# Kernel tuning notes

Measured on AMD Instinct MI355X. Metric: run time of the kernel, lower is better.

Reference implementation:

```python
import jax, jax.numpy as jnp
import numpy as np

B, T, K = 512, 512, 128
START, STOP = K - 2, K - 1
NEG = -10000.0


def setup_inputs() -> dict:
    key = jax.random.key(0)
    k1, k2, k3 = jax.random.split(key, 3)
    feats = jax.random.normal(k1, (B, T, K), dtype=jnp.float32)
    # gold tags exclude START/STOP
    tags = jax.random.randint(k2, (B, T), 0, K - 2)
    transitions = jax.random.normal(k3, (K, K), dtype=jnp.float32)
    # __init__ pins: transitions[START, :] = -10000 ; transitions[:, STOP] = -10000
    transitions = transitions.at[START, :].set(NEG).at[:, STOP].set(NEG)
    return {"feats": feats, "tags": tags, "transitions": transitions}


def _forward_alg(feats, transitions):
    # feats: [B, T, K]; CRF partition function via log-space semiring scan
    Bb, Tt, Kk = feats.shape
    alpha0 = jnp.full((Bb, Kk), NEG, dtype=feats.dtype).at[:, START].set(0.0)

    def step(alpha, feat):  # alpha: [B, K_prev], feat: [B, K_next]
        # score[b, next, prev] = alpha[b, prev] + T[next, prev] + feat[b, next]
        s = alpha[:, None, :] + transitions[None, :, :] + feat[:, :, None]
        return jax.nn.logsumexp(s, axis=-1), None

    alpha, _ = jax.lax.scan(step, alpha0, jnp.swapaxes(feats, 0, 1))
    return jax.nn.logsumexp(alpha + transitions[STOP], axis=-1)  # [B]


def _score_sentence(feats, tags, transitions):
    # score of the gold path, fully vectorized over time
    Bb = feats.shape[0]
    start = jnp.full((Bb, 1), START, dtype=tags.dtype)
    ext = jnp.concatenate([start, tags], axis=1)  # [B, T+1]
    trans_score = transitions[ext[:, 1:], ext[:, :-1]].sum(axis=1)  # [B]
    emit_score = jnp.take_along_axis(feats, tags[:, :, None], axis=2)[..., 0].sum(axis=1)
    return trans_score + emit_score + transitions[STOP, ext[:, -1]]


def reference(feats, tags, transitions):
    # neg_log_likelihood: mean over batch of (log Z - gold path score)
    forward_score = _forward_alg(feats, transitions)
    gold_score = _score_sentence(feats, tags, transitions)
    return jnp.sum(forward_score - gold_score) / feats.shape[0]
```

## Files before the change

kernel.cpp:

```cpp
#include <hip/hip_runtime.h>
#include <math.h>

#define Bb 512
#define Tt 512
#define Kk 128
#define NSTART 126
#define NSTOP  127
#define PW 32
#define NTHR 256

static constexpr float LOG2E = 1.4426950408889634f;
static constexpr float LN2   = 0.6931471805599453f;

__device__ __forceinline__ float fexp2(float x) {
  return __builtin_amdgcn_exp2f(x);
}
__device__ __forceinline__ float flog2(float x) {
  return __builtin_amdgcn_logf(x);
}

__global__ __launch_bounds__(NTHR, 2) void crf_nll_lin2(
    const float* __restrict__ feats,
    const int*   __restrict__ tags,
    const float* __restrict__ trans,
    float* __restrict__ part)
{
  const int b   = blockIdx.x;
  const int tid = threadIdx.x;
  const int q   = tid & 3;
  const int nb  = tid >> 2;
  const int n0  = nb;
  const int n1  = nb + 64;
  const int w   = tid >> 6;

  __shared__ __align__(16) float aL[2][4][Kk];
  __shared__ float red[4];

  float E0[PW], E1[PW];
  {
    const float* t0 = trans + (size_t)n0 * Kk + q * PW;
    const float* t1 = trans + (size_t)n1 * Kk + q * PW;
    #pragma unroll
    for (int j = 0; j < PW; j += 4) {
      float4 v0 = *(const float4*)(t0 + j);
      float4 v1 = *(const float4*)(t1 + j);
      E0[j+0] = fexp2(v0.x * LOG2E);
      E0[j+1] = fexp2(v0.y * LOG2E);
      E0[j+2] = fexp2(v0.z * LOG2E);
      E0[j+3] = fexp2(v0.w * LOG2E);
      E1[j+0] = fexp2(v1.x * LOG2E);
      E1[j+1] = fexp2(v1.y * LOG2E);
      E1[j+2] = fexp2(v1.z * LOG2E);
      E1[j+3] = fexp2(v1.w * LOG2E);
    }
  }
  #pragma unroll
  for (int j = 0; j < PW; ++j) {
    asm volatile("" : "+v"(E0[j]), "+v"(E1[j]));
  }

  aL[0][q][(n0 - 8*q) & (Kk-1)] = (n0 == NSTART) ? 1.0f : 0.0f;
  aL[0][q][(n1 - 8*q) & (Kk-1)] = (n1 == NSTART) ? 1.0f : 0.0f;
  __syncthreads();

  const float* fb = feats + (size_t)b * Tt * Kk;
  float C2 = 0.0f;
  float f0 = fb[n0], f1 = fb[n1];

  for (int t = 0; t < Tt; ++t) {
    const int cur = t & 1;
    float f0n = 0.f, f1n = 0.f;
    if (t + 1 < Tt) {
      f0n = fb[(size_t)(t + 1) * Kk + n0];
      f1n = fb[(size_t)(t + 1) * Kk + n1];
    }

    const float* ap = &aL[cur][q][q * 24];
    float a0=0.f,a1=0.f,a2=0.f,a3=0.f, c0=0.f,c1=0.f,c2=0.f,c3=0.f;
    #pragma unroll
    for (int j4 = 0; j4 < PW/4; ++j4) {
      const float4 av = *(const float4*)(ap + j4*4);
      a0 = fmaf(E0[4*j4+0], av.x, a0);
      a1 = fmaf(E0[4*j4+1], av.y, a1);
      a2 = fmaf(E0[4*j4+2], av.z, a2);
      a3 = fmaf(E0[4*j4+3], av.w, a3);
      c0 = fmaf(E1[4*j4+0], av.x, c0);
      c1 = fmaf(E1[4*j4+1], av.y, c1);
      c2 = fmaf(E1[4*j4+2], av.z, c2);
      c3 = fmaf(E1[4*j4+3], av.w, c3);
    }
    float s0 = (a0 + a1) + (a2 + a3);
    float s1 = (c0 + c1) + (c2 + c3);
    s0 += __shfl_xor(s0, 1, 64);
    s0 += __shfl_xor(s0, 2, 64);
    s1 += __shfl_xor(s1, 1, 64);
    s1 += __shfl_xor(s1, 2, 64);
    float y0 = fexp2(f0 * LOG2E) * s0;
    float y1 = fexp2(f1 * LOG2E) * s1;

    if ((t & 3) == 3) {
      float m = fmaxf(y0, y1);
      m = fmaxf(m, __shfl_xor(m, 4, 64));
      m = fmaxf(m, __shfl_xor(m, 8, 64));
      m = fmaxf(m, __shfl_xor(m, 16, 64));
      m = fmaxf(m, __shfl_xor(m, 32, 64));
      if ((tid & 63) == 0) red[w] = m;
      __syncthreads();
      m = fmaxf(fmaxf(red[0], red[1]), fmaxf(red[2], red[3]));
      C2 += flog2(m);
      float inv = 1.0f / m;
      y0 *= inv; y1 *= inv;
    }

    const int nxt = cur ^ 1;
    aL[nxt][q][(n0 - 8*q) & (Kk-1)] = y0;
    aL[nxt][q][(n1 - 8*q) & (Kk-1)] = y1;
    __syncthreads();
    f0 = f0n; f1 = f1n;
  }

  float v = 0.0f;
  if (tid < Kk) {
    float es = fexp2(trans[(size_t)NSTOP * Kk + tid] * LOG2E);
    v = aL[0][0][tid] * es;
  }
  #pragma unroll
  for (int off = 32; off >= 1; off >>= 1) v += __shfl_xor(v, off, 64);
  if ((tid & 63) == 0) red[w] = v;
  __syncthreads();
  const float S = (red[0] + red[1]) + (red[2] + red[3]);
  const float fwd = LN2 * (C2 + flog2(S));

  __syncthreads();
  const int* tg = tags + (size_t)b * Tt;
  float g = 0.0f;
  #pragma unroll
  for (int k2 = 0; k2 < Tt / NTHR; ++k2) {
    const int tt  = tid + k2 * NTHR;
    const int curt = tg[tt];
    const int prv  = (tt == 0) ? NSTART : tg[tt - 1];
    g += trans[(size_t)curt * Kk + prv] + fb[(size_t)tt * Kk + curt];
  }
  if (tid == 0) g += trans[(size_t)NSTOP * Kk + tg[Tt - 1]];
  #pragma unroll
  for (int off = 32; off >= 1; off >>= 1) g += __shfl_xor(g, off, 64);
  if ((tid & 63) == 0) red[w] = g;
  __syncthreads();
  const float gold = (red[0] + red[1]) + (red[2] + red[3]);

  if (tid == 0) part[b] = fwd - gold;
}

__global__ __launch_bounds__(256) void reduce_mean_kernel(
    const float* __restrict__ part, float* __restrict__ out)
{
  __shared__ float buf[4];
  const int tid = threadIdx.x;
  float v = part[tid] + part[tid + 256];
  #pragma unroll
  for (int off = 32; off >= 1; off >>= 1) v += __shfl_xor(v, off, 64);
  if ((tid & 63) == 0) buf[tid >> 6] = v;
  __syncthreads();
  if (tid == 0)
    out[0] = (buf[0] + buf[1] + buf[2] + buf[3]) * (1.0f / (float)Bb);
}

extern "C" void kernel_launch(void* const* d_in, const int* in_sizes, int n_in,
                              void* d_out, int out_size, void* d_ws, size_t ws_size,
                              hipStream_t stream) {
  const float* feats = (const float*)d_in[0];
  const int*   tags  = (const int*)d_in[1];
  const float* trans = (const float*)d_in[2];
  float* part = (float*)d_ws;

  crf_nll_lin2<<<dim3(Bb), dim3(NTHR), 0, stream>>>(feats, tags, trans, part);
  reduce_mean_kernel<<<dim3(1), dim3(256), 0, stream>>>(part, (float*)d_out);
}
```

Before: 256.5 us.

## Halve threads per sequence, four next-states per thread, DPP quad reductions

Shrinks each block from 256 to 128 threads (2 waves), so each thread now owns four next-tag rows of exp(transitions) in registers (128 floats) instead of two. Each LDS float4 load of alpha is now reused across four rows, and the per-step barrier spans only two waves. The quad partial-sum reduction switches from ds_swizzle-style shuffles to DPP quad_perm adds, and the division becomes a hardware reciprocal. The cost is much higher register pressure and fewer waves per sequence, so the latency of the serial recurrence is less hidden.

```diff
diff --git a/kernel.cpp b/kernel.cpp
--- a/kernel.cpp
+++ b/kernel.cpp
@@ -6,20 +6,29 @@
 #define Kk 128
 #define NSTART 126
 #define NSTOP  127
+#define NTHR 128
+#define RN 4
+#define QS 4
 #define PW 32
-#define NTHR 256
 
 static constexpr float LOG2E = 1.4426950408889634f;
 static constexpr float LN2   = 0.6931471805599453f;
 
-__device__ __forceinline__ float fexp2(float x) {
-  return __builtin_amdgcn_exp2f(x);
+__device__ __forceinline__ float fexp2(float x) { return __builtin_amdgcn_exp2f(x); }
+__device__ __forceinline__ float flog2(float x) { return __builtin_amdgcn_logf(x); }
+__device__ __forceinline__ float frcp (float x) { return __builtin_amdgcn_rcpf(x); }
+
+template <int CTRL>
+__device__ __forceinline__ float dpp_qp_add(float s) {
+  union { float f; int i; } a, r;
+  a.f = s;
+  r.i = __builtin_amdgcn_update_dpp(a.i, a.i, CTRL, 0xf, 0xf, false);
+  return s + r.f;
 }
-__device__ __forceinline__ float flog2(float x) {
-  return __builtin_amdgcn_logf(x);
-}
+#define QP_XOR1 0xB1
+#define QP_XOR2 0x4E
 
-__global__ __launch_bounds__(NTHR, 2) void crf_nll_lin2(
+__global__ __launch_bounds__(NTHR, 1) void crf_nll_lin3(
     const float* __restrict__ feats,
     const int*   __restrict__ tags,
     const float* __restrict__ trans,
@@ -29,114 +38,118 @@
   const int tid = threadIdx.x;
   const int q   = tid & 3;
   const int nb  = tid >> 2;
-  const int n0  = nb;
-  const int n1  = nb + 64;
   const int w   = tid >> 6;
 
-  __shared__ __align__(16) float aL[2][4][Kk];
-  __shared__ float red[4];
+  __shared__ __align__(16) float aL[2][QS][Kk];
+  __shared__ float red[2];
 
-  float E0[PW], E1[PW];
-  {
-    const float* t0 = trans + (size_t)n0 * Kk + q * PW;
-    const float* t1 = trans + (size_t)n1 * Kk + q * PW;
+  float E[RN][PW];
+  #pragma unroll
+  for (int r = 0; r < RN; ++r) {
+    const float* tr = trans + (size_t)(nb + 32*r) * Kk + q * PW;
     #pragma unroll
     for (int j = 0; j < PW; j += 4) {
-      float4 v0 = *(const float4*)(t0 + j);
-      float4 v1 = *(const float4*)(t1 + j);
-      E0[j+0] = fexp2(v0.x * LOG2E);
-      E0[j+1] = fexp2(v0.y * LOG2E);
-      E0[j+2] = fexp2(v0.z * LOG2E);
-      E0[j+3] = fexp2(v0.w * LOG2E);
-      E1[j+0] = fexp2(v1.x * LOG2E);
-      E1[j+1] = fexp2(v1.y * LOG2E);
-      E1[j+2] = fexp2(v1.z * LOG2E);
-      E1[j+3] = fexp2(v1.w * LOG2E);
+      float4 v = *(const float4*)(tr + j);
+      E[r][j+0] = fexp2(v.x * LOG2E);
+      E[r][j+1] = fexp2(v.y * LOG2E);
+      E[r][j+2] = fexp2(v.z * LOG2E);
+      E[r][j+3] = fexp2(v.w * LOG2E);
     }
   }
   #pragma unroll
-  for (int j = 0; j < PW; ++j) {
-    asm volatile("" : "+v"(E0[j]), "+v"(E1[j]));
-  }
+  for (int r = 0; r < RN; ++r)
+    #pragma unroll
+    for (int j = 0; j < PW; ++j)
+      asm volatile("" : "+v"(E[r][j]));
 
-  aL[0][q][(n0 - 8*q) & (Kk-1)] = (n0 == NSTART) ? 1.0f : 0.0f;
-  aL[0][q][(n1 - 8*q) & (Kk-1)] = (n1 == NSTART) ? 1.0f : 0.0f;
+  int wi[RN];
+  #pragma unroll
+  for (int r = 0; r < RN; ++r) wi[r] = ((nb + 32*r) - 8*q) & (Kk - 1);
+
+  #pragma unroll
+  for (int r = 0; r < RN; ++r)
+    aL[0][q][wi[r]] = ((nb + 32*r) == NSTART) ? 1.0f : 0.0f;
   __syncthreads();
 
   const float* fb = feats + (size_t)b * Tt * Kk;
   float C2 = 0.0f;
-  float f0 = fb[n0], f1 = fb[n1];
+  float f[RN], fn[RN];
+  #pragma unroll
+  for (int r = 0; r < RN; ++r) f[r] = fb[nb + 32*r] * LOG2E;
 
   for (int t = 0; t < Tt; ++t) {
     const int cur = t & 1;
-    float f0n = 0.f, f1n = 0.f;
     if (t + 1 < Tt) {
-      f0n = fb[(size_t)(t + 1) * Kk + n0];
-      f1n = fb[(size_t)(t + 1) * Kk + n1];
+      #pragma unroll
+      for (int r = 0; r < RN; ++r)
+        fn[r] = fb[(size_t)(t + 1) * Kk + nb + 32*r] * LOG2E;
+    } else {
+      #pragma unroll
+      for (int r = 0; r < RN; ++r) fn[r] = 0.0f;
     }
 
     const float* ap = &aL[cur][q][q * 24];
-    float a0=0.f,a1=0.f,a2=0.f,a3=0.f, c0=0.f,c1=0.f,c2=0.f,c3=0.f;
+    float acc[RN][4];
+    #pragma unroll
+    for (int r = 0; r < RN; ++r)
+      #pragma unroll
+      for (int c = 0; c < 4; ++c) acc[r][c] = 0.0f;
     #pragma unroll
     for (int j4 = 0; j4 < PW/4; ++j4) {
-      const float4 av = *(const float4*)(ap + j4*4);
-      a0 = fmaf(E0[4*j4+0], av.x, a0);
-      a1 = fmaf(E0[4*j4+1], av.y, a1);
-      a2 = fmaf(E0[4*j4+2], av.z, a2);
-      a3 = fmaf(E0[4*j4+3], av.w, a3);
-      c0 = fmaf(E1[4*j4+0], av.x, c0);
-      c1 = fmaf(E1[4*j4+1], av.y, c1);
-      c2 = fmaf(E1[4*j4+2], av.z, c2);
-      c3 = fmaf(E1[4*j4+3], av.w, c3);
+      const float4 av = *(const float4*)(ap + 4*j4);
+      #pragma unroll
+      for (int r = 0; r < RN; ++r) {
+        acc[r][0] = fmaf(E[r][4*j4+0], av.x, acc[r][0]);
+        acc[r][1] = fmaf(E[r][4*j4+1], av.y, acc[r][1]);
+        acc[r][2] = fmaf(E[r][4*j4+2], av.z, acc[r][2]);
+        acc[r][3] = fmaf(E[r][4*j4+3], av.w, acc[r][3]);
+      }
     }
-    float s0 = (a0 + a1) + (a2 + a3);
-    float s1 = (c0 + c1) + (c2 + c3);
-    s0 += __shfl_xor(s0, 1, 64);
-    s0 += __shfl_xor(s0, 2, 64);
-    s1 += __shfl_xor(s1, 1, 64);
-    s1 += __shfl_xor(s1, 2, 64);
-    float y0 = fexp2(f0 * LOG2E) * s0;
-    float y1 = fexp2(f1 * LOG2E) * s1;
+    float y[RN];
+    #pragma unroll
+    for (int r = 0; r < RN; ++r) {
+      float s = (acc[r][0] + acc[r][1]) + (acc[r][2] + acc[r][3]);
+      s = dpp_qp_add<QP_XOR1>(s);
+      s = dpp_qp_add<QP_XOR2>(s);
+      y[r] = fexp2(f[r]) * s;
+    }
 
     if ((t & 3) == 3) {
-      float m = fmaxf(y0, y1);
+      float m = fmaxf(fmaxf(y[0], y[1]), fmaxf(y[2], y[3]));
       m = fmaxf(m, __shfl_xor(m, 4, 64));
       m = fmaxf(m, __shfl_xor(m, 8, 64));
       m = fmaxf(m, __shfl_xor(m, 16, 64));
       m = fmaxf(m, __shfl_xor(m, 32, 64));
       if ((tid & 63) == 0) red[w] = m;
       __syncthreads();
-      m = fmaxf(fmaxf(red[0], red[1]), fmaxf(red[2], red[3]));
+      m = fmaxf(red[0], red[1]);
       C2 += flog2(m);
-      float inv = 1.0f / m;
-      y0 *= inv; y1 *= inv;
+      const float inv = frcp(m);
+      #pragma unroll
+      for (int r = 0; r < RN; ++r) y[r] *= inv;
     }
 
     const int nxt = cur ^ 1;
-    aL[nxt][q][(n0 - 8*q) & (Kk-1)] = y0;
-    aL[nxt][q][(n1 - 8*q) & (Kk-1)] = y1;
+    #pragma unroll
+    for (int r = 0; r < RN; ++r) aL[nxt][q][wi[r]] = y[r];
     __syncthreads();
-    f0 = f0n; f1 = f1n;
+    #pragma unroll
+    for (int r = 0; r < RN; ++r) f[r] = fn[r];
   }
 
-  float v = 0.0f;
-  if (tid < Kk) {
-    float es = fexp2(trans[(size_t)NSTOP * Kk + tid] * LOG2E);
-    v = aL[0][0][tid] * es;
-  }
+  float v = aL[0][0][tid] * fexp2(trans[(size_t)NSTOP * Kk + tid] * LOG2E);
   #pragma unroll
   for (int off = 32; off >= 1; off >>= 1) v += __shfl_xor(v, off, 64);
   if ((tid & 63) == 0) red[w] = v;
   __syncthreads();
-  const float S = (red[0] + red[1]) + (red[2] + red[3]);
-  const float fwd = LN2 * (C2 + flog2(S));
+  const float fwd = LN2 * (C2 + flog2(red[0] + red[1]));
 
   __syncthreads();
   const int* tg = tags + (size_t)b * Tt;
   float g = 0.0f;
   #pragma unroll
   for (int k2 = 0; k2 < Tt / NTHR; ++k2) {
-    const int tt  = tid + k2 * NTHR;
+    const int tt   = tid + k2 * NTHR;
     const int curt = tg[tt];
     const int prv  = (tt == 0) ? NSTART : tg[tt - 1];
     g += trans[(size_t)curt * Kk + prv] + fb[(size_t)tt * Kk + curt];
@@ -146,7 +159,7 @@
   for (int off = 32; off >= 1; off >>= 1) g += __shfl_xor(g, off, 64);
   if ((tid & 63) == 0) red[w] = g;
   __syncthreads();
-  const float gold = (red[0] + red[1]) + (red[2] + red[3]);
+  const float gold = red[0] + red[1];
 
   if (tid == 0) part[b] = fwd - gold;
 }
@@ -173,6 +186,6 @@
   const float* trans = (const float*)d_in[2];
   float* part = (float*)d_ws;
 
-  crf_nll_lin2<<<dim3(Bb), dim3(NTHR), 0, stream>>>(feats, tags, trans, part);
+  crf_nll_lin3<<<dim3(Bb), dim3(NTHR), 0, stream>>>(feats, tags, trans, part);
   reduce_mean_kernel<<<dim3(1), dim3(256), 0, stream>>>(part, (float*)d_out);
 }
```

Measured after the change: 381.6 us. +48.8%, slower.

## Store alpha vector in bf16 shared memory and use DPP quad reductions

Applied to the files above, without the earlier changes.

Replaces the per-quad padded fp32 alpha buffer with one packed bf16 buffer, so each thread loads half as many shared-memory bytes per step and only two lanes write. The quad partial-sum shuffles become DPP quad-permute adds, division becomes a hardware reciprocal, and the LOG2E scaling of feats is folded into the prefetch. Rounding alpha to bf16 every step reduces precision of the partition function and may affect accuracy, and the unpadded layout could introduce LDS bank conflicts.

```diff
diff --git a/kernel.cpp b/kernel.cpp
--- a/kernel.cpp
+++ b/kernel.cpp
@@ -6,20 +6,38 @@
 #define Kk 128
 #define NSTART 126
 #define NSTOP  127
+#define NTHR 256
 #define PW 32
-#define NTHR 256
 
 static constexpr float LOG2E = 1.4426950408889634f;
 static constexpr float LN2   = 0.6931471805599453f;
 
-__device__ __forceinline__ float fexp2(float x) {
-  return __builtin_amdgcn_exp2f(x);
-}
-__device__ __forceinline__ float flog2(float x) {
-  return __builtin_amdgcn_logf(x);
-}
-
-__global__ __launch_bounds__(NTHR, 2) void crf_nll_lin2(
+__device__ __forceinline__ float fexp2(float x) { return __builtin_amdgcn_exp2f(x); }
+__device__ __forceinline__ float flog2(float x) { return __builtin_amdgcn_logf(x); }
+__device__ __forceinline__ float frcp (float x) { return __builtin_amdgcn_rcpf(x); }
+
+template <int CTRL>
+__device__ __forceinline__ float dpp_qp_add(float s) {
+  union { float f; int i; } a, r;
+  a.f = s;
+  r.i = __builtin_amdgcn_update_dpp(a.i, a.i, CTRL, 0xf, 0xf, false);
+  return s + r.f;
+}
+#define QP_XOR1 0xB1
+#define QP_XOR2 0x4E
+
+__device__ __forceinline__ float bf16lo(unsigned int d) {
+  union { unsigned int u; float f; } v; v.u = d << 16;        return v.f;
+}
+__device__ __forceinline__ float bf16hi(unsigned int d) {
+  union { unsigned int u; float f; } v; v.u = d & 0xFFFF0000u; return v.f;
+}
+__device__ __forceinline__ unsigned short to_bf16(float x) {
+  union { float f; unsigned int u; } v; v.f = x;
+  return (unsigned short)((v.u + 0x8000u) >> 16);
+}
+
+__global__ __launch_bounds__(NTHR, 2) void crf_nll_bf16(
     const float* __restrict__ feats,
     const int*   __restrict__ tags,
     const float* __restrict__ trans,
@@ -29,74 +47,76 @@
   const int tid = threadIdx.x;
   const int q   = tid & 3;
   const int nb  = tid >> 2;
-  const int n0  = nb;
-  const int n1  = nb + 64;
   const int w   = tid >> 6;
 
-  __shared__ __align__(16) float aL[2][4][Kk];
+  __shared__ __align__(16) unsigned int aU[2][Kk/2];
   __shared__ float red[4];
 
   float E0[PW], E1[PW];
   {
-    const float* t0 = trans + (size_t)n0 * Kk + q * PW;
-    const float* t1 = trans + (size_t)n1 * Kk + q * PW;
+    const float* t0 = trans + (size_t)nb * Kk + q * PW;
+    const float* t1 = trans + (size_t)(nb + 64) * Kk + q * PW;
     #pragma unroll
     for (int j = 0; j < PW; j += 4) {
       float4 v0 = *(const float4*)(t0 + j);
       float4 v1 = *(const float4*)(t1 + j);
-      E0[j+0] = fexp2(v0.x * LOG2E);
-      E0[j+1] = fexp2(v0.y * LOG2E);
-      E0[j+2] = fexp2(v0.z * LOG2E);
-      E0[j+3] = fexp2(v0.w * LOG2E);
-      E1[j+0] = fexp2(v1.x * LOG2E);
-      E1[j+1] = fexp2(v1.y * LOG2E);
-      E1[j+2] = fexp2(v1.z * LOG2E);
-      E1[j+3] = fexp2(v1.w * LOG2E);
-    }
-  }
-  #pragma unroll
-  for (int j = 0; j < PW; ++j) {
+      E0[j+0] = fexp2(v0.x * LOG2E);  E0[j+1] = fexp2(v0.y * LOG2E);
+      E0[j+2] = fexp2(v0.z * LOG2E);  E0[j+3] = fexp2(v0.w * LOG2E);
+      E1[j+0] = fexp2(v1.x * LOG2E);  E1[j+1] = fexp2(v1.y * LOG2E);
+      E1[j+2] = fexp2(v1.z * LOG2E);  E1[j+3] = fexp2(v1.w * LOG2E);
+    }
+  }
+  #pragma unroll
+  for (int j = 0; j < PW; ++j)
     asm volatile("" : "+v"(E0[j]), "+v"(E1[j]));
-  }
-
-  aL[0][q][(n0 - 8*q) & (Kk-1)] = (n0 == NSTART) ? 1.0f : 0.0f;
-  aL[0][q][(n1 - 8*q) & (Kk-1)] = (n1 == NSTART) ? 1.0f : 0.0f;
+
+  if (tid < Kk/2) aU[0][tid] = (tid == 63) ? 0x00003F80u : 0u;
   __syncthreads();
 
   const float* fb = feats + (size_t)b * Tt * Kk;
   float C2 = 0.0f;
-  float f0 = fb[n0], f1 = fb[n1];
+  float f0 = fb[nb] * LOG2E, f1 = fb[nb + 64] * LOG2E;
 
   for (int t = 0; t < Tt; ++t) {
     const int cur = t & 1;
     float f0n = 0.f, f1n = 0.f;
     if (t + 1 < Tt) {
-      f0n = fb[(size_t)(t + 1) * Kk + n0];
-      f1n = fb[(size_t)(t + 1) * Kk + n1];
-    }
-
-    const float* ap = &aL[cur][q][q * 24];
+      f0n = fb[(size_t)(t + 1) * Kk + nb] * LOG2E;
+      f1n = fb[(size_t)(t + 1) * Kk + nb + 64] * LOG2E;
+    }
+
+    const uint4* ap = (const uint4*)&aU[cur][q * (PW/2)];
+    uint4 av[4];
+    #pragma unroll
+    for (int j4 = 0; j4 < 4; ++j4) av[j4] = ap[j4];
+
     float a0=0.f,a1=0.f,a2=0.f,a3=0.f, c0=0.f,c1=0.f,c2=0.f,c3=0.f;
     #pragma unroll
-    for (int j4 = 0; j4 < PW/4; ++j4) {
-      const float4 av = *(const float4*)(ap + j4*4);
-      a0 = fmaf(E0[4*j4+0], av.x, a0);
-      a1 = fmaf(E0[4*j4+1], av.y, a1);
-      a2 = fmaf(E0[4*j4+2], av.z, a2);
-      a3 = fmaf(E0[4*j4+3], av.w, a3);
-      c0 = fmaf(E1[4*j4+0], av.x, c0);
-      c1 = fmaf(E1[4*j4+1], av.y, c1);
-      c2 = fmaf(E1[4*j4+2], av.z, c2);
-      c3 = fmaf(E1[4*j4+3], av.w, c3);
+    for (int j4 = 0; j4 < 4; ++j4) {
+      const unsigned int d[4] = { av[j4].x, av[j4].y, av[j4].z, av[j4].w };
+      #pragma unroll
+      for (int k = 0; k < 4; ++k) {
+        const int j = j4*8 + k*2;
+        const float lo = bf16lo(d[k]);
+        const float hi = bf16hi(d[k]);
+        a0 = fmaf(E0[j+0], lo, a0);
+        a1 = fmaf(E0[j+1], hi, a1);
+        c0 = fmaf(E1[j+0], lo, c0);
+        c1 = fmaf(E1[j+1], hi, c1);
+        { float tmp = a0; a0 = a2; a2 = tmp; }
+        { float tmp = a1; a1 = a3; a3 = tmp; }
+        { float tmp = c0; c0 = c2; c2 = tmp; }
+        { float tmp = c1; c1 = c3; c3 = tmp; }
+      }
     }
     float s0 = (a0 + a1) + (a2 + a3);
     float s1 = (c0 + c1) + (c2 + c3);
-    s0 += __shfl_xor(s0, 1, 64);
-    s0 += __shfl_xor(s0, 2, 64);
-    s1 += __shfl_xor(s1, 1, 64);
-    s1 += __shfl_xor(s1, 2, 64);
-    float y0 = fexp2(f0 * LOG2E) * s0;
-    float y1 = fexp2(f1 * LOG2E) * s1;
+    s0 = dpp_qp_add<QP_XOR1>(s0);
+    s0 = dpp_qp_add<QP_XOR2>(s0);
+    s1 = dpp_qp_add<QP_XOR1>(s1);
+    s1 = dpp_qp_add<QP_XOR2>(s1);
+    float y0 = fexp2(f0) * s0;
+    float y1 = fexp2(f1) * s1;
 
     if ((t & 3) == 3) {
       float m = fmaxf(y0, y1);
@@ -108,21 +128,23 @@
       __syncthreads();
       m = fmaxf(fmaxf(red[0], red[1]), fmaxf(red[2], red[3]));
       C2 += flog2(m);
-      float inv = 1.0f / m;
+      const float inv = frcp(m);
       y0 *= inv; y1 *= inv;
     }
 
     const int nxt = cur ^ 1;
-    aL[nxt][q][(n0 - 8*q) & (Kk-1)] = y0;
-    aL[nxt][q][(n1 - 8*q) & (Kk-1)] = y1;
+    unsigned short* aH = (unsigned short*)&aU[nxt][0];
+    if (q == 0) aH[nb]      = to_bf16(y0);
+    if (q == 1) aH[nb + 64] = to_bf16(y1);
     __syncthreads();
     f0 = f0n; f1 = f1n;
   }
 
   float v = 0.0f;
   if (tid < Kk) {
-    float es = fexp2(trans[(size_t)NSTOP * Kk + tid] * LOG2E);
-    v = aL[0][0][tid] * es;
+    const unsigned int d = aU[0][tid >> 1];
+    const float an = (tid & 1) ? bf16hi(d) : bf16lo(d);
+    v = an * fexp2(trans[(size_t)NSTOP * Kk + tid] * LOG2E);
   }
   #pragma unroll
   for (int off = 32; off >= 1; off >>= 1) v += __shfl_xor(v, off, 64);
@@ -136,7 +158,7 @@
   float g = 0.0f;
   #pragma unroll
   for (int k2 = 0; k2 < Tt / NTHR; ++k2) {
-    const int tt  = tid + k2 * NTHR;
+    const int tt   = tid + k2 * NTHR;
     const int curt = tg[tt];
     const int prv  = (tt == 0) ? NSTART : tg[tt - 1];
     g += trans[(size_t)curt * Kk + prv] + fb[(size_t)tt * Kk + curt];
@@ -173,6 +195,6 @@
   const float* trans = (const float*)d_in[2];
   float* part = (float*)d_ws;
 
-  crf_nll_lin2<<<dim3(Bb), dim3(NTHR), 0, stream>>>(feats, tags, trans, part);
+  crf_nll_bf16<<<dim3(Bb), dim3(NTHR), 0, stream>>>(feats, tags, trans, part);
   reduce_mean_kernel<<<dim3(1), dim3(256), 0, stream>>>(part, (float*)d_out);
 }
```

Result: slower. 278.3 us (+8.5%).

## Use packed fp16 dot2 recurrence with per-step deferred max normalization

Applied to the files above, without the earlier changes.

Stores the exponentiated transition matrix and the alpha vector as packed fp16 pairs and computes the recurrence with v_dot2_f32_f16, which halves the LDS footprint and the multiply-add count. The max normalization now runs every step: each wave writes its partial max to a double-buffered slot that is consumed at the next step, removing the extra barrier that the every-fourth-step rescale needed. Quad and row reductions use DPP moves instead of shuffles, and feature loads are prefetched two steps ahead. The cost is reduced precision in alpha and transitions; fp16 range and rounding could introduce error in the log partition function.

```diff
diff --git a/kernel.cpp b/kernel.cpp
--- a/kernel.cpp
+++ b/kernel.cpp
@@ -6,20 +6,39 @@
 #define Kk 128
 #define NSTART 126
 #define NSTOP  127
-#define PW 32
 #define NTHR 256
 
 static constexpr float LOG2E = 1.4426950408889634f;
 static constexpr float LN2   = 0.6931471805599453f;
 
-__device__ __forceinline__ float fexp2(float x) {
-  return __builtin_amdgcn_exp2f(x);
+__device__ __forceinline__ float fexp2(float x){ return __builtin_amdgcn_exp2f(x); }
+__device__ __forceinline__ float flog2(float x){ return __builtin_amdgcn_logf(x); }
+
+__device__ __forceinline__ void dot2a(float& acc, unsigned e, unsigned a){
+  asm("v_dot2_f32_f16 %0, %1, %2, %0" : "+v"(acc) : "v"(e), "v"(a));
 }
-__device__ __forceinline__ float flog2(float x) {
-  return __builtin_amdgcn_logf(x);
+__device__ __forceinline__ unsigned pkh(float lo, float hi){
+  union { _Float16 h[2]; unsigned u; } p;
+  p.h[0] = (_Float16)lo; p.h[1] = (_Float16)hi;
+  return p.u;
 }
+__device__ __forceinline__ float cvth(unsigned u){
+  float f; asm("v_cvt_f32_f16 %0, %1" : "=v"(f) : "v"(u)); return f;
+}
+template<int CTRL>
+__device__ __forceinline__ float dpp_mov(float s){
+  union {float f; int i;} a, r; a.f = s;
+  r.i = __builtin_amdgcn_update_dpp(a.i, a.i, CTRL, 0xf, 0xf, false);
+  return r.f;
+}
+#define QP_XOR1  0xB1
+#define QP_XOR2  0x4E
+#define ROW_ROR4 0x124
+#define ROW_ROR8 0x128
 
-__global__ __launch_bounds__(NTHR, 2) void crf_nll_lin2(
+__global__ __attribute__((amdgpu_flat_work_group_size(NTHR, NTHR),
+                          amdgpu_waves_per_eu(2, 2)))
+void crf_v13(
     const float* __restrict__ feats,
     const int*   __restrict__ tags,
     const float* __restrict__ trans,
@@ -29,104 +48,94 @@
   const int tid = threadIdx.x;
   const int q   = tid & 3;
   const int nb  = tid >> 2;
-  const int n0  = nb;
-  const int n1  = nb + 64;
   const int w   = tid >> 6;
+  const int l   = tid & 63;
 
-  __shared__ __align__(16) float aL[2][4][Kk];
+  __shared__ __align__(16) unsigned aW[2][64];
+  __shared__ __align__(16) float Mp[2][4];
   __shared__ float red[4];
 
-  float E0[PW], E1[PW];
+  unsigned E0[16], E1[16];
   {
-    const float* t0 = trans + (size_t)n0 * Kk + q * PW;
-    const float* t1 = trans + (size_t)n1 * Kk + q * PW;
+    const float* t0 = trans + (size_t)nb * Kk;
+    const float* t1 = trans + (size_t)(nb + 64) * Kk;
     #pragma unroll
-    for (int j = 0; j < PW; j += 4) {
-      float4 v0 = *(const float4*)(t0 + j);
-      float4 v1 = *(const float4*)(t1 + j);
-      E0[j+0] = fexp2(v0.x * LOG2E);
-      E0[j+1] = fexp2(v0.y * LOG2E);
-      E0[j+2] = fexp2(v0.z * LOG2E);
-      E0[j+3] = fexp2(v0.w * LOG2E);
-      E1[j+0] = fexp2(v1.x * LOG2E);
-      E1[j+1] = fexp2(v1.y * LOG2E);
-      E1[j+2] = fexp2(v1.z * LOG2E);
-      E1[j+3] = fexp2(v1.w * LOG2E);
+    for (int j = 0; j < 16; ++j) {
+      const int d = 16*q + j;
+      E0[j] = pkh(fexp2(t0[d] * LOG2E), fexp2(t0[d + 64] * LOG2E));
+      E1[j] = pkh(fexp2(t1[d] * LOG2E), fexp2(t1[d + 64] * LOG2E));
     }
   }
   #pragma unroll
-  for (int j = 0; j < PW; ++j) {
+  for (int j = 0; j < 16; ++j)
     asm volatile("" : "+v"(E0[j]), "+v"(E1[j]));
-  }
 
-  aL[0][q][(n0 - 8*q) & (Kk-1)] = (n0 == NSTART) ? 1.0f : 0.0f;
-  aL[0][q][(n1 - 8*q) & (Kk-1)] = (n1 == NSTART) ? 1.0f : 0.0f;
+  if (tid < 64) aW[0][tid] = (tid == 62) ? 0x3C000000u : 0u;
+  if (tid < 4)  Mp[0][tid] = 1.0f;
   __syncthreads();
 
   const float* fb = feats + (size_t)b * Tt * Kk;
+  float f0  = fb[nb],       f1  = fb[nb + 64];
+  float f0n = fb[Kk + nb],  f1n = fb[Kk + nb + 64];
   float C2 = 0.0f;
-  float f0 = fb[n0], f1 = fb[n1];
 
   for (int t = 0; t < Tt; ++t) {
-    const int cur = t & 1;
-    float f0n = 0.f, f1n = 0.f;
-    if (t + 1 < Tt) {
-      f0n = fb[(size_t)(t + 1) * Kk + n0];
-      f1n = fb[(size_t)(t + 1) * Kk + n1];
+    const int cur = t & 1, nxt = cur ^ 1;
+
+    const float4 mp4 = *reinterpret_cast<const float4*>(&Mp[cur][0]);
+    const float mm = fmaxf(fmaxf(mp4.x, mp4.y), fmaxf(mp4.z, mp4.w));
+    const float lm = flog2(mm);
+    C2 += lm + 6.0f;
+    const float lsc = -6.0f - lm;
+
+    const uint4* ap = reinterpret_cast<const uint4*>(&aW[cur][16 * q]);
+    uint4 av0 = ap[0], av1 = ap[1], av2 = ap[2], av3 = ap[3];
+
+    float A0=0.f,A1=0.f,A2=0.f,A3=0.f, C0=0.f,C1=0.f,C2_=0.f,C3=0.f;
+#define D4(AV, J)                                              \
+    dot2a(A0, E0[J+0], AV.x);  dot2a(C0, E1[J+0], AV.x);       \
+    dot2a(A1, E0[J+1], AV.y);  dot2a(C1, E1[J+1], AV.y);       \
+    dot2a(A2, E0[J+2], AV.z);  dot2a(C2_, E1[J+2], AV.z);      \
+    dot2a(A3, E0[J+3], AV.w);  dot2a(C3, E1[J+3], AV.w);
+    D4(av0, 0) D4(av1, 4) D4(av2, 8) D4(av3, 12)
+#undef D4
+    float s0 = (A0 + A1) + (A2 + A3);
+    float s1 = (C0 + C1) + (C2_ + C3);
+    s0 = s0 + dpp_mov<QP_XOR1>(s0);
+    s0 = s0 + dpp_mov<QP_XOR2>(s0);
+    s1 = s1 + dpp_mov<QP_XOR1>(s1);
+    s1 = s1 + dpp_mov<QP_XOR2>(s1);
+
+    const float y0 = s0 * fexp2(fmaf(f0, LOG2E, lsc));
+    const float y1 = s1 * fexp2(fmaf(f1, LOG2E, lsc));
+
+    f0 = f0n; f1 = f1n;
+    {
+      int tn = t + 2; if (tn > Tt - 1) tn = Tt - 1;
+      f0n = fb[(size_t)tn * Kk + nb];
+      f1n = fb[(size_t)tn * Kk + nb + 64];
     }
 
-    const float* ap = &aL[cur][q][q * 24];
-    float a0=0.f,a1=0.f,a2=0.f,a3=0.f, c0=0.f,c1=0.f,c2=0.f,c3=0.f;
-    #pragma unroll
-    for (int j4 = 0; j4 < PW/4; ++j4) {
-      const float4 av = *(const float4*)(ap + j4*4);
-      a0 = fmaf(E0[4*j4+0], av.x, a0);
-      a1 = fmaf(E0[4*j4+1], av.y, a1);
-      a2 = fmaf(E0[4*j4+2], av.z, a2);
-      a3 = fmaf(E0[4*j4+3], av.w, a3);
-      c0 = fmaf(E1[4*j4+0], av.x, c0);
-      c1 = fmaf(E1[4*j4+1], av.y, c1);
-      c2 = fmaf(E1[4*j4+2], av.z, c2);
-      c3 = fmaf(E1[4*j4+3], av.w, c3);
-    }
-    float s0 = (a0 + a1) + (a2 + a3);
-    float s1 = (c0 + c1) + (c2 + c3);
-    s0 += __shfl_xor(s0, 1, 64);
-    s0 += __shfl_xor(s0, 2, 64);
-    s1 += __shfl_xor(s1, 1, 64);
-    s1 += __shfl_xor(s1, 2, 64);
-    float y0 = fexp2(f0 * LOG2E) * s0;
-    float y1 = fexp2(f1 * LOG2E) * s1;
+    float pm = fmaxf(y0, y1);
+    pm = fmaxf(pm, dpp_mov<ROW_ROR4>(pm));
+    pm = fmaxf(pm, dpp_mov<ROW_ROR8>(pm));
+    pm = fmaxf(pm, __shfl_xor(pm, 16, 64));
+    pm = fmaxf(pm, __shfl_xor(pm, 32, 64));
+    if (l == 0) Mp[nxt][w] = pm;
 
-    if ((t & 3) == 3) {
-      float m = fmaxf(y0, y1);
-      m = fmaxf(m, __shfl_xor(m, 4, 64));
-      m = fmaxf(m, __shfl_xor(m, 8, 64));
-      m = fmaxf(m, __shfl_xor(m, 16, 64));
-      m = fmaxf(m, __shfl_xor(m, 32, 64));
-      if ((tid & 63) == 0) red[w] = m;
-      __syncthreads();
-      m = fmaxf(fmaxf(red[0], red[1]), fmaxf(red[2], red[3]));
-      C2 += flog2(m);
-      float inv = 1.0f / m;
-      y0 *= inv; y1 *= inv;
-    }
-
-    const int nxt = cur ^ 1;
-    aL[nxt][q][(n0 - 8*q) & (Kk-1)] = y0;
-    aL[nxt][q][(n1 - 8*q) & (Kk-1)] = y1;
+    if (q == 0) aW[nxt][nb] = pkh(y0, y1);
     __syncthreads();
-    f0 = f0n; f1 = f1n;
   }
 
   float v = 0.0f;
-  if (tid < Kk) {
-    float es = fexp2(trans[(size_t)NSTOP * Kk + tid] * LOG2E);
-    v = aL[0][0][tid] * es;
+  if (tid < 64) {
+    const unsigned d = aW[0][tid];
+    v = cvth(d)       * fexp2(trans[(size_t)NSTOP * Kk + tid]      * LOG2E)
+      + cvth(d >> 16) * fexp2(trans[(size_t)NSTOP * Kk + tid + 64] * LOG2E);
   }
   #pragma unroll
   for (int off = 32; off >= 1; off >>= 1) v += __shfl_xor(v, off, 64);
-  if ((tid & 63) == 0) red[w] = v;
+  if (l == 0) red[w] = v;
   __syncthreads();
   const float S = (red[0] + red[1]) + (red[2] + red[3]);
   const float fwd = LN2 * (C2 + flog2(S));
@@ -136,7 +145,7 @@
   float g = 0.0f;
   #pragma unroll
   for (int k2 = 0; k2 < Tt / NTHR; ++k2) {
-    const int tt  = tid + k2 * NTHR;
+    const int tt   = tid + k2 * NTHR;
     const int curt = tg[tt];
     const int prv  = (tt == 0) ? NSTART : tg[tt - 1];
     g += trans[(size_t)curt * Kk + prv] + fb[(size_t)tt * Kk + curt];
@@ -144,7 +153,7 @@
   if (tid == 0) g += trans[(size_t)NSTOP * Kk + tg[Tt - 1]];
   #pragma unroll
   for (int off = 32; off >= 1; off >>= 1) g += __shfl_xor(g, off, 64);
-  if ((tid & 63) == 0) red[w] = g;
+  if (l == 0) red[w] = g;
   __syncthreads();
   const float gold = (red[0] + red[1]) + (red[2] + red[3]);
 
@@ -173,6 +182,6 @@
   const float* trans = (const float*)d_in[2];
   float* part = (float*)d_ws;
 
-  crf_nll_lin2<<<dim3(Bb), dim3(NTHR), 0, stream>>>(feats, tags, trans, part);
+  crf_v13<<<dim3(Bb), dim3(NTHR), 0, stream>>>(feats, tags, trans, part);
   reduce_mean_kernel<<<dim3(1), dim3(256), 0, stream>>>(part, (float*)d_out);
 }
```

Measured after the change: 266.9 us. +4.0%, slower.
